# Performance work log

Hardware: AMD Instinct MI355X
Metric: run time of the kernel (lower is better)

Reference implementation:

```python
import jax, jax.numpy as jnp
from jax import lax
import numpy as np

BETA = 0.5       # leak factor of snn.Leaky
THR = 1.0        # firing threshold
SLOPE = 25.0     # fast_sigmoid surrogate slope (snntorch default)
NUM_STEPS = 16

@jax.custom_vjp
def spike(m):
    # Heaviside of (mem - threshold); surrogate grad = 1/(slope*|m|+1)^2
    return (m > 0).astype(m.dtype)

def _spike_fwd(m):
    return spike(m), m

def _spike_bwd(m, g):
    return (g / (SLOPE * jnp.abs(m) + 1.0) ** 2,)

spike.defvjp(_spike_fwd, _spike_bwd)


def setup_inputs() -> dict:
    key = jax.random.key(0)
    k1, k2, k3 = jax.random.split(key, 3)
    x = jax.random.uniform(k1, (4096, 1, 28, 28), dtype=jnp.float32)
    conv_w = jax.random.normal(k2, (8, 1, 3, 3), dtype=jnp.float32) * 0.3
    fc_w = jax.random.normal(k3, (10, 1352), dtype=jnp.float32) * 0.05
    return {"x": x, "conv_w": conv_w, "fc_w": fc_w}


def reference(x, conv_w, fc_w):
    B = x.shape[0]
    # conv1(x) is identical every timestep -> compute once (same math).
    cur1 = lax.conv_general_dilated(
        x, conv_w, window_strides=(1, 1), padding='VALID',
        dimension_numbers=('NCHW', 'OIHW', 'NCHW'))  # [B,8,26,26]

    mem1_0 = jnp.zeros_like(cur1)
    mem2_0 = jnp.zeros((B, 10), dtype=x.dtype)

    def step(carry, _):
        mem1, mem2 = carry
        # LIF layer 1: integrate, fire, subtract-reset (reset detached)
        mem1 = BETA * mem1 + cur1
        spk1 = spike(mem1 - THR)
        mem1 = mem1 - lax.stop_gradient(spk1) * THR
        # avg pool 2x2 -> [B,8,13,13]
        pool = spk1.reshape(B, 8, 13, 2, 13, 2).mean(axis=(3, 5))
        # fc (no bias): [B,1352] @ [1352,10]
        cur2 = pool.reshape(B, -1) @ fc_w.T
        # LIF layer 2
        mem2 = BETA * mem2 + cur2
        spk2 = spike(mem2 - THR)
        mem2 = mem2 - lax.stop_gradient(spk2) * THR
        return (mem1, mem2), spk2

    (_, _), spk2_rec = lax.scan(step, (mem1_0, mem2_0), None, length=NUM_STEPS)
    return spk2_rec.sum(axis=0)  # [B,10] spike counts
```

## Files before the change

kernel.cpp:

```cpp
#include <hip/hip_runtime.h>


typedef float v2f __attribute__((ext_vector_type(2)));
typedef float f32x4 __attribute__((ext_vector_type(4)));
typedef short s16x8 __attribute__((ext_vector_type(8)));

#if __has_builtin(__builtin_elementwise_fma)
#define VFMA(a, b, c) __builtin_elementwise_fma((a), (b), (c))
#else
#define VFMA(a, b, c) ((a) * (b) + (c))
#endif

#define NU 6
#define KS 43
#define SPLITS 4

__device__ __forceinline__ unsigned short bf16_rne(float f) {
    unsigned u = __float_as_uint(f);
    return (unsigned short)((u + 0x7FFFu + ((u >> 16) & 1u)) >> 16);
}
__device__ __forceinline__ float bf16_back(unsigned short h) {
    return __uint_as_float(((unsigned)h) << 16);
}

__global__ void build_bfrag_kernel(const float* __restrict__ fc_w,
                                   s16x8* __restrict__ wsfrag) {
    const int blk = blockIdx.x;
    const int p   = blk / KS;
    const int ks  = blk - p * KS;
    const int l   = threadIdx.x;
    s16x8 frag;
    #pragma unroll
    for (int jj = 0; jj < 8; ++jj) {
        const int k = ks * 32 + (l >> 4) * 8 + jj;
        const int n = l & 15;
        float r = (k < 1352 && n < 10) ? 0.25f * fc_w[n * 1352 + k] : 0.0f;
        unsigned short b = 0;
        for (int q = 0; q <= p; ++q) {
            b = bf16_rne(r);
            r -= bf16_back(b);
        }
        frag[jj] = (short)b;
    }
    wsfrag[blk * 64 + l] = frag;
}

__global__ __launch_bounds__(256, 3) void snn_fused_kernel(
    const float* __restrict__ x,
    const float* __restrict__ conv_w,
    const s16x8* __restrict__ wsfrag,
    float* __restrict__ out)
{
    const int b    = blockIdx.x;
    const int tid  = threadIdx.x;
    const int lane = tid & 63;
    const int wid  = tid >> 6;

    __shared__ unsigned short sA[KS * 544];
    __shared__ float scC[4 * 256];
    __shared__ float scw[72];
    __shared__ float scur2[160];

    if (tid < 72) scw[tid] = conv_w[tid];

    int xbase[NU], kbase[NU], sbase[NU];
    #pragma unroll
    for (int i = 0; i < NU; ++i) {
        const int u      = tid + 256 * i;
        const bool valid = (u < 1352);
        const int uu  = valid ? u : 0;
        const int k   = uu / 169;
        const int rem = uu - k * 169;
        const int pr  = rem / 13;
        const int pc  = rem - pr * 13;
        xbase[i] = 56 * pr + 2 * pc;
        kbase[i] = 9 * k;
        const int uo = u & 31;
        sbase[i] = (u >> 5) * 544 + (uo >> 3) * 136 + (uo & 7);
    }
    __syncthreads();

    const float* xb = x + (size_t)b * 784;
    v2f cur2[NU][2];
    v2f mem2[NU][2];
    #pragma unroll
    for (int i = 0; i < NU; ++i) {
        float cw[9];
        #pragma unroll
        for (int qq = 0; qq < 9; ++qq) cw[qq] = scw[kbase[i] + qq];

        float xr[4][4];
        #pragma unroll
        for (int r = 0; r < 4; ++r) {
            const float2* rp = reinterpret_cast<const float2*>(xb + xbase[i] + 28 * r);
            const float2 a = rp[0], c2 = rp[1];
            xr[r][0] = a.x; xr[r][1] = a.y; xr[r][2] = c2.x; xr[r][3] = c2.y;
        }

        const bool valid = (tid + 256 * i) < 1352;
        float cell[2][2];
        #pragma unroll
        for (int dr = 0; dr < 2; ++dr)
            #pragma unroll
            for (int dc = 0; dc < 2; ++dc) {
                float acc = 0.0f;
                #pragma unroll
                for (int ki = 0; ki < 3; ++ki)
                    #pragma unroll
                    for (int kj = 0; kj < 3; ++kj)
                        acc += xr[dr + ki][dc + kj] * cw[ki * 3 + kj];
                cell[dr][dc] = valid ? acc : 0.0f;
            }
        cur2[i][0] = (v2f){cell[0][0], cell[0][1]};
        cur2[i][1] = (v2f){cell[1][0], cell[1][1]};
        mem2[i][0] = (v2f){0.0f, 0.0f};
        mem2[i][1] = (v2f){0.0f, 0.0f};
    }

    const v2f half2 = (v2f){0.5f, 0.5f};

    #pragma unroll
    for (int t = 0; t < 16; ++t) {
        #pragma unroll
        for (int i = 0; i < NU; ++i) {
            v2f m01 = VFMA(half2, mem2[i][0], cur2[i][0]);
            v2f m23 = VFMA(half2, mem2[i][1], cur2[i][1]);
            v2f sp01, sp23;
            sp01.x = m01.x > 1.0f ? 1.0f : 0.0f;
            sp01.y = m01.y > 1.0f ? 1.0f : 0.0f;
            sp23.x = m23.x > 1.0f ? 1.0f : 0.0f;
            sp23.y = m23.y > 1.0f ? 1.0f : 0.0f;
            mem2[i][0] = m01 - sp01;
            mem2[i][1] = m23 - sp23;
            v2f s = sp01 + sp23;
            const float c = s.x + s.y;
            const unsigned short cb = (unsigned short)(__float_as_uint(c) >> 16);
            if (i < 5 || tid < 96)
                sA[sbase[i] + t * 8] = cb;
        }
    }
    __syncthreads();

    {
        const int p = wid;
        f32x4 acc = (f32x4){0.f, 0.f, 0.f, 0.f};
        const int arow = (lane >> 4) * 136 + (lane & 15) * 8;
        #pragma unroll 2
        for (int ks = 0; ks < KS; ++ks) {
            const s16x8 a  = *reinterpret_cast<const s16x8*>(&sA[ks * 544 + arow]);
            const s16x8 bw = wsfrag[(p * KS + ks) * 64 + lane];
            acc = __builtin_amdgcn_mfma_f32_16x16x32_bf16(a, bw, acc, 0, 0, 0);
        }
        const int o = lane & 15;
        #pragma unroll
        for (int r = 0; r < 4; ++r) {
            const int t = (lane >> 4) * 4 + r;
            scC[wid * 256 + t * 16 + o] = acc[r];
        }
    }
    __syncthreads();

    if (tid < 160) {
        const int t = tid / 10;
        const int o = tid - t * 10;
        const int idx = t * 16 + o;
        scur2[tid] = (scC[idx] + scC[256 + idx]) + (scC[512 + idx] + scC[768 + idx]);
    }
    __syncthreads();

    if (tid < 10) {
        float m2 = 0.0f, cnt = 0.0f;
        #pragma unroll
        for (int t = 0; t < 16; ++t) {
            m2 = __builtin_fmaf(0.5f, m2, scur2[t * 10 + tid]);
            float ms = m2 - 1.0f;
            bool  sp = ms > 0.0f;
            m2  = sp ? ms : m2;
            cnt += sp ? 1.0f : 0.0f;
        }
        out[(size_t)b * 10 + tid] = cnt;
    }
}

extern "C" void kernel_launch(void* const* d_in, const int* in_sizes, int n_in,
                              void* d_out, int out_size, void* d_ws, size_t ws_size,
                              hipStream_t stream) {
    const float* x      = (const float*)d_in[0];
    const float* conv_w = (const float*)d_in[1];
    const float* fc_w   = (const float*)d_in[2];
    float* out          = (float*)d_out;
    s16x8* wsfrag       = (s16x8*)d_ws;

    build_bfrag_kernel<<<SPLITS * KS, 64, 0, stream>>>(fc_w, wsfrag);

    const int B = in_sizes[0] / 784;
    snn_fused_kernel<<<B, 256, 0, stream>>>(x, conv_w, wsfrag, out);
}
```

Baseline: 76.35 us.

## Assign 8 consecutive pooled units per thread and pack spike writes into 16-byte LDS stores

Each of 169 threads now handles 8 consecutive pooled units instead of 6 strided ones. Each timestep's 8 bf16 spike counts are packed with byte-perm into one 128-bit shared-memory store, replacing 6 scalar 16-bit stores. Three extra threads zero the K-padding region. This cuts LDS store instructions but leaves 87 threads idle during the conv/LIF phase and raises per-thread register pressure.

```diff
diff --git a/kernel.cpp b/kernel.cpp
--- a/kernel.cpp
+++ b/kernel.cpp
@@ -11,7 +11,7 @@
 #define VFMA(a, b, c) ((a) * (b) + (c))
 #endif
 
-#define NU 6
+#define NU 8
 #define KS 43
 #define SPLITS 4
 
@@ -21,6 +21,15 @@
 }
 __device__ __forceinline__ float bf16_back(unsigned short h) {
     return __uint_as_float(((unsigned)h) << 16);
+}
+
+__device__ __forceinline__ unsigned bf16pair(float flo, float fhi) {
+#if __has_builtin(__builtin_amdgcn_perm)
+    return __builtin_amdgcn_perm(__float_as_uint(fhi), __float_as_uint(flo),
+                                 0x07060302u);
+#else
+    return (__float_as_uint(fhi) & 0xFFFF0000u) | (__float_as_uint(flo) >> 16);
+#endif
 }
 
 __global__ void build_bfrag_kernel(const float* __restrict__ fc_w,
@@ -56,88 +65,99 @@
     const int lane = tid & 63;
     const int wid  = tid >> 6;
 
-    __shared__ unsigned short sA[KS * 544];
+    __shared__ __align__(16) unsigned short sA[KS * 544];
     __shared__ float scC[4 * 256];
     __shared__ float scw[72];
     __shared__ float scur2[160];
 
     if (tid < 72) scw[tid] = conv_w[tid];
 
-    int xbase[NU], kbase[NU], sbase[NU];
-    #pragma unroll
-    for (int i = 0; i < NU; ++i) {
-        const int u      = tid + 256 * i;
-        const bool valid = (u < 1352);
-        const int uu  = valid ? u : 0;
-        const int k   = uu / 169;
-        const int rem = uu - k * 169;
-        const int pr  = rem / 13;
-        const int pc  = rem - pr * 13;
-        xbase[i] = 56 * pr + 2 * pc;
-        kbase[i] = 9 * k;
-        const int uo = u & 31;
-        sbase[i] = (u >> 5) * 544 + (uo >> 3) * 136 + (uo & 7);
-    }
-    __syncthreads();
-
-    const float* xb = x + (size_t)b * 784;
     v2f cur2[NU][2];
     v2f mem2[NU][2];
-    #pragma unroll
-    for (int i = 0; i < NU; ++i) {
-        float cw[9];
-        #pragma unroll
-        for (int qq = 0; qq < 9; ++qq) cw[qq] = scw[kbase[i] + qq];
-
-        float xr[4][4];
-        #pragma unroll
-        for (int r = 0; r < 4; ++r) {
-            const float2* rp = reinterpret_cast<const float2*>(xb + xbase[i] + 28 * r);
-            const float2 a = rp[0], c2 = rp[1];
-            xr[r][0] = a.x; xr[r][1] = a.y; xr[r][2] = c2.x; xr[r][3] = c2.y;
-        }
-
-        const bool valid = (tid + 256 * i) < 1352;
-        float cell[2][2];
-        #pragma unroll
-        for (int dr = 0; dr < 2; ++dr)
-            #pragma unroll
-            for (int dc = 0; dc < 2; ++dc) {
-                float acc = 0.0f;
+    int sbyte = (tid >> 2) * 1088 + (tid & 3) * 272;
+
+    int xbase[NU], kbase[NU];
+    if (tid < 169) {
+        #pragma unroll
+        for (int i = 0; i < NU; ++i) {
+            const int u   = tid * 8 + i;
+            const int k   = u / 169;
+            const int rem = u - k * 169;
+            const int pr  = rem / 13;
+            const int pc  = rem - pr * 13;
+            xbase[i] = 56 * pr + 2 * pc;
+            kbase[i] = 9 * k;
+        }
+    }
+    __syncthreads();
+
+    if (tid < 169) {
+        const float* xb = x + (size_t)b * 784;
+        #pragma unroll
+        for (int i = 0; i < NU; ++i) {
+            float cw[9];
+            #pragma unroll
+            for (int qq = 0; qq < 9; ++qq) cw[qq] = scw[kbase[i] + qq];
+
+            float xr[4][4];
+            #pragma unroll
+            for (int r = 0; r < 4; ++r) {
+                const float2* rp = reinterpret_cast<const float2*>(xb + xbase[i] + 28 * r);
+                const float2 a = rp[0], c2 = rp[1];
+                xr[r][0] = a.x; xr[r][1] = a.y; xr[r][2] = c2.x; xr[r][3] = c2.y;
+            }
+
+            float cell[2][2];
+            #pragma unroll
+            for (int dr = 0; dr < 2; ++dr)
                 #pragma unroll
-                for (int ki = 0; ki < 3; ++ki)
+                for (int dc = 0; dc < 2; ++dc) {
+                    float acc = 0.0f;
                     #pragma unroll
-                    for (int kj = 0; kj < 3; ++kj)
-                        acc += xr[dr + ki][dc + kj] * cw[ki * 3 + kj];
-                cell[dr][dc] = valid ? acc : 0.0f;
+                    for (int ki = 0; ki < 3; ++ki)
+                        #pragma unroll
+                        for (int kj = 0; kj < 3; ++kj)
+                            acc += xr[dr + ki][dc + kj] * cw[ki * 3 + kj];
+                    cell[dr][dc] = acc;
+                }
+            cur2[i][0] = (v2f){cell[0][0], cell[0][1]};
+            cur2[i][1] = (v2f){cell[1][0], cell[1][1]};
+            mem2[i][0] = (v2f){0.0f, 0.0f};
+            mem2[i][1] = (v2f){0.0f, 0.0f};
+        }
+
+        const v2f half2 = (v2f){0.5f, 0.5f};
+        #pragma unroll
+        for (int t = 0; t < 16; ++t) {
+            float c[NU];
+            #pragma unroll
+            for (int i = 0; i < NU; ++i) {
+                v2f m01 = VFMA(half2, mem2[i][0], cur2[i][0]);
+                v2f m23 = VFMA(half2, mem2[i][1], cur2[i][1]);
+                v2f sp01, sp23;
+                sp01.x = m01.x > 1.0f ? 1.0f : 0.0f;
+                sp01.y = m01.y > 1.0f ? 1.0f : 0.0f;
+                sp23.x = m23.x > 1.0f ? 1.0f : 0.0f;
+                sp23.y = m23.y > 1.0f ? 1.0f : 0.0f;
+                mem2[i][0] = m01 - sp01;
+                mem2[i][1] = m23 - sp23;
+                v2f s = sp01 + sp23;
+                c[i] = s.x + s.y;
             }
-        cur2[i][0] = (v2f){cell[0][0], cell[0][1]};
-        cur2[i][1] = (v2f){cell[1][0], cell[1][1]};
-        mem2[i][0] = (v2f){0.0f, 0.0f};
-        mem2[i][1] = (v2f){0.0f, 0.0f};
-    }
-
-    const v2f half2 = (v2f){0.5f, 0.5f};
-
-    #pragma unroll
-    for (int t = 0; t < 16; ++t) {
-        #pragma unroll
-        for (int i = 0; i < NU; ++i) {
-            v2f m01 = VFMA(half2, mem2[i][0], cur2[i][0]);
-            v2f m23 = VFMA(half2, mem2[i][1], cur2[i][1]);
-            v2f sp01, sp23;
-            sp01.x = m01.x > 1.0f ? 1.0f : 0.0f;
-            sp01.y = m01.y > 1.0f ? 1.0f : 0.0f;
-            sp23.x = m23.x > 1.0f ? 1.0f : 0.0f;
-            sp23.y = m23.y > 1.0f ? 1.0f : 0.0f;
-            mem2[i][0] = m01 - sp01;
-            mem2[i][1] = m23 - sp23;
-            v2f s = sp01 + sp23;
-            const float c = s.x + s.y;
-            const unsigned short cb = (unsigned short)(__float_as_uint(c) >> 16);
-            if (i < 5 || tid < 96)
-                sA[sbase[i] + t * 8] = cb;
-        }
+            uint4 w;
+            w.x = bf16pair(c[0], c[1]);
+            w.y = bf16pair(c[2], c[3]);
+            w.z = bf16pair(c[4], c[5]);
+            w.w = bf16pair(c[6], c[7]);
+            *reinterpret_cast<uint4*>(
+                reinterpret_cast<char*>(sA) + sbyte + t * 16) = w;
+        }
+    } else if (tid < 172) {
+        const uint4 z = (uint4){0u, 0u, 0u, 0u};
+        #pragma unroll
+        for (int t = 0; t < 16; ++t)
+            *reinterpret_cast<uint4*>(
+                reinterpret_cast<char*>(sA) + sbyte + t * 16) = z;
     }
     __syncthreads();
 
```

New measurement: 95.01 us. +24.4%, slower.
